# Kernel optimization log

Measured on AMD Instinct MI355X. Metric: run time of the kernel, lower is better.

Reference implementation:

```python
import jax, jax.numpy as jnp
import numpy as np

DIM = 256; HEADS = 8; HD = 32; WS = 3; LOCAL = WS * WS; SR = 4


def _unfold(x, ws):
    # x: (B, c, H, W) -> (B, c, ws*ws, H*W), zero padding (matches nn.Unfold)
    p = ws // 2
    B, c, H, W = x.shape
    xp = jnp.pad(x, ((0, 0), (0, 0), (p, p), (p, p)))
    pat = jnp.stack([xp[:, :, i:i + H, j:j + W] for i in range(ws) for j in range(ws)], axis=2)
    return pat.reshape(B, c, ws * ws, H * W)


def _l2norm(x):
    return x / jnp.sqrt(jnp.sum(x * x, axis=-1, keepdims=True) + 1e-12)


def setup_inputs():
    key = jax.random.key(0)
    ks = jax.random.split(key, 16)
    B, H, W, C, h, d = 4, 64, 64, DIM, HEADS, HD
    N = H * W; pH, pW = H // SR, W // SR; PL = pH * pW; L = 1024
    s = 0.02
    inp = {}
    inp["x"] = jax.random.normal(ks[0], (B, N, C), jnp.float32)
    inp["relative_coords_table"] = jax.random.uniform(ks[1], (L, 2), jnp.float32, -1.0, 1.0)
    inp["relative_pos_index"] = jax.random.randint(ks[2], (N, PL), 0, L)
    inp["q_w"] = jax.random.normal(ks[3], (C, C), jnp.float32) * s
    inp["q_b"] = jnp.zeros((C,), jnp.float32)
    inp["kv_w"] = jax.random.normal(ks[4], (C, 2 * C), jnp.float32) * s
    inp["kv_b"] = jnp.zeros((2 * C,), jnp.float32)
    inp["temperature"] = jnp.log(jnp.expm1(jnp.ones((h, 1, 1), jnp.float32) / 0.24))
    inp["query_embedding"] = jax.random.normal(ks[5], (h, 1, d), jnp.float32) * s
    inp["sr_w"] = jax.random.normal(ks[6], (C, C), jnp.float32) * s
    inp["sr_b"] = jnp.zeros((C,), jnp.float32)
    inp["norm_g"] = jnp.ones((C,), jnp.float32)
    inp["norm_b"] = jnp.zeros((C,), jnp.float32)
    inp["cpb1_w"] = jax.random.normal(ks[7], (2, 512), jnp.float32) * s
    inp["cpb1_b"] = jnp.zeros((512,), jnp.float32)
    inp["cpb2_w"] = jax.random.normal(ks[8], (512, h), jnp.float32) * s
    inp["cpb2_b"] = jnp.zeros((h,), jnp.float32)
    inp["rpb_local"] = jax.random.normal(ks[9], (h, LOCAL), jnp.float32) * 0.0004
    inp["learnable_tokens"] = jax.random.normal(ks[10], (h, d, LOCAL), jnp.float32) * s
    inp["learnable_bias"] = jnp.zeros((h, 1, LOCAL), jnp.float32)
    inp["proj_w"] = jax.random.normal(ks[11], (C, C), jnp.float32) * s
    inp["proj_b"] = jnp.zeros((C,), jnp.float32)
    inp["H"] = H
    inp["W"] = W
    return inp


def _forward(x, relative_coords_table, relative_pos_index, q_w, q_b, kv_w, kv_b,
             temperature, query_embedding, sr_w, sr_b, norm_g, norm_b,
             cpb1_w, cpb1_b, cpb2_w, cpb2_b, rpb_local, learnable_tokens,
             learnable_bias, proj_w, proj_b, H, W):
    B, N, C = x.shape
    h, d = HEADS, HD
    pH, pW = H // SR, W // SR
    PL = pH * pW

    # static buffers: per-pixel valid-neighbor count, log seq-length scale, padding mask
    uf1 = _unfold(jnp.ones((1, 1, H, W), jnp.float32), WS)[0, 0]   # (LOCAL, N)
    counts = uf1.sum(axis=0)[:, None]                               # (N, 1)
    seq_scale = jnp.log(counts + PL)                                # (N, 1)
    pad_mask = (uf1.T == 0)                                         # (N, LOCAL)

    q = (x @ q_w + q_b).reshape(B, N, h, d).transpose(0, 2, 1, 3)   # (B,h,N,d)
    q_norm = _l2norm(q)
    q_scaled = (q_norm + query_embedding) * jax.nn.softplus(temperature) * seq_scale

    kv = (x @ kv_w + kv_b).reshape(B, N, 2 * h, d).transpose(0, 2, 1, 3)
    k_local, v_local = kv[:, :h], kv[:, h:]                         # (B,h,N,d)

    # --- local branch: sliding-window QK^T + learned relative bias ---
    kn = _l2norm(k_local)
    k_img = kn.transpose(0, 1, 3, 2).reshape(B, h * d, H, W)
    k_uf = _unfold(k_img, WS).reshape(B, h, d, LOCAL, N)            # (B,h,d,l,N)
    attn_local = jnp.einsum('bhnd,bhdln->bhnl', q_scaled, k_uf) + rpb_local[None, :, None, :]
    attn_local = jnp.where(pad_mask[None, None], jnp.float32(-1e9), attn_local)

    # --- pooled global branch ---
    xs = jax.nn.gelu(x @ sr_w + sr_b, approximate=False)            # 1x1 conv + GELU
    xs = xs.reshape(B, pH, SR, pW, SR, C).mean(axis=(2, 4)).reshape(B, PL, C)
    mu = xs.mean(-1, keepdims=True)
    var = ((xs - mu) ** 2).mean(-1, keepdims=True)
    xs = (xs - mu) / jnp.sqrt(var + 1e-5) * norm_g + norm_b         # LayerNorm

    kvp = (xs @ kv_w + kv_b).reshape(B, PL, 2 * h, d).transpose(0, 2, 1, 3)
    k_pool, v_pool = kvp[:, :h], kvp[:, h:]
    kp = _l2norm(k_pool)

    # MLP-generated continuous relative position bias
    t = jax.nn.relu(relative_coords_table @ cpb1_w + cpb1_b) @ cpb2_w + cpb2_b  # (L,h)
    pool_bias = t.T[:, relative_pos_index.reshape(-1)].reshape(h, N, PL)

    attn_pool = jnp.einsum('bhnd,bhpd->bhnp', q_scaled, kp) + pool_bias[None]

    # joint softmax over [local | pool]
    attn = jax.nn.softmax(jnp.concatenate([attn_local, attn_pool], axis=-1), axis=-1)
    attn_local, attn_pool = attn[..., :LOCAL], attn[..., LOCAL:]

    # learnable-token refinement of local weights
    attn_local = jnp.einsum('bhnd,hdl->bhnl', q_norm, learnable_tokens) + learnable_bias[None] + attn_local

    v_img = v_local.transpose(0, 1, 3, 2).reshape(B, h * d, H, W)
    v_uf = _unfold(v_img, WS).reshape(B, h, d, LOCAL, N)            # zero-padded V
    x_local = jnp.einsum('bhnl,bhdln->bhnd', attn_local, v_uf)
    x_pool = jnp.einsum('bhnp,bhpd->bhnd', attn_pool, v_pool)

    out = (x_local + x_pool).transpose(0, 2, 1, 3).reshape(B, N, C)
    return out @ proj_w + proj_b


def reference(x, relative_coords_table, relative_pos_index, q_w, q_b, kv_w, kv_b,
              temperature, query_embedding, sr_w, sr_b, norm_g, norm_b,
              cpb1_w, cpb1_b, cpb2_w, cpb2_b, rpb_local, learnable_tokens,
              learnable_bias, proj_w, proj_b, H, W):
    return _forward(x, relative_coords_table, relative_pos_index, q_w, q_b, kv_w, kv_b,
                    temperature, query_embedding, sr_w, sr_b, norm_g, norm_b,
                    cpb1_w, cpb1_b, cpb2_w, cpb2_b, rpb_local, learnable_tokens,
                    learnable_bias, proj_w, proj_b, H, W)
```

## Files before the change

kernel.cpp:

```cpp
#include <hip/hip_runtime.h>
#include <math.h>

#define B_   4
#define N_   4096
#define C_   256
#define NH   8
#define D_   32
#define PL_  256
#define IMG  64

typedef __attribute__((ext_vector_type(8))) short short8b;
typedef __attribute__((ext_vector_type(4))) float f32x4;
typedef unsigned short ushort_t;

__device__ __forceinline__ ushort_t f2bf(float f) {
    unsigned u = __float_as_uint(f);
    u += 0x7FFFu + ((u >> 16) & 1u);
    return (ushort_t)(u >> 16);
}
__device__ __forceinline__ float bf2f(ushort_t s) {
    return __uint_as_float(((unsigned)s) << 16);
}
__device__ __forceinline__ unsigned pk2(float lo, float hi) {
    return (unsigned)f2bf(lo) | ((unsigned)f2bf(hi) << 16);
}
__device__ __forceinline__ float gelu_f(float v) {
    return 0.5f * v * (1.0f + erff(v * 0.70710678118654752440f));
}

__global__ __launch_bounds__(256) void prep_all(const float* __restrict__ x,
                                                const float* __restrict__ q_w,
                                                const float* __restrict__ kv_w,
                                                const float* __restrict__ sr_w,
                                                const float* __restrict__ p_w,
                                                const float* __restrict__ rct,
                                                const float* __restrict__ c1w,
                                                const float* __restrict__ c1b,
                                                const float* __restrict__ c2w,
                                                const float* __restrict__ c2b,
                                                ushort_t* __restrict__ x_bf,
                                                ushort_t* __restrict__ WTall,
                                                ushort_t* __restrict__ pwT,
                                                float* __restrict__ tT)
{
    const int blk = blockIdx.x;
    const int tid = threadIdx.x;
    if (blk < 2048) {
        int gid = blk * 256 + tid;
        const float4* p = (const float4*)(x + (size_t)gid * 8);
        float4 v0 = p[0], v1 = p[1];
        short8b o;
        o[0]=(short)f2bf(v0.x); o[1]=(short)f2bf(v0.y);
        o[2]=(short)f2bf(v0.z); o[3]=(short)f2bf(v0.w);
        o[4]=(short)f2bf(v1.x); o[5]=(short)f2bf(v1.y);
        o[6]=(short)f2bf(v1.z); o[7]=(short)f2bf(v1.w);
        *(short8b*)&x_bf[(size_t)gid * 8] = o;
    } else if (blk < 2208) {
        int wt = (blk - 2048) * 256 + tid;
        int row = wt >> 5;
        int k0  = (wt & 31) << 3;
        const float* W; int N, n; ushort_t* dst;
        if (row < 256)       { W = q_w;  N = 256; n = row;        dst = WTall + (size_t)row * 256; }
        else if (row < 768)  { W = kv_w; N = 512; n = row - 256;  dst = WTall + (size_t)row * 256; }
        else if (row < 1024) { W = sr_w; N = 256; n = row - 768;  dst = WTall + (size_t)row * 256; }
        else                 { W = p_w;  N = 256; n = row - 1024; dst = pwT + (size_t)(row-1024) * 256; }
        short8b v;
        #pragma unroll
        for (int j = 0; j < 8; ++j) v[j] = (short)f2bf(W[(size_t)(k0 + j) * N + n]);
        *(short8b*)&dst[k0] = v;
    } else {
        int l = (blk - 2208) * 4 + (tid >> 6);
        int lane = tid & 63;
        float c0 = rct[l*2+0], c1 = rct[l*2+1];
        float acc[8] = {0,0,0,0,0,0,0,0};
        for (int j = lane; j < 512; j += 64) {
            float hv = fmaxf(c0 * c1w[j] + c1 * c1w[512+j] + c1b[j], 0.f);
            #pragma unroll
            for (int hh = 0; hh < 8; ++hh) acc[hh] += hv * c2w[j*8 + hh];
        }
        #pragma unroll
        for (int o = 32; o > 0; o >>= 1)
            #pragma unroll
            for (int hh = 0; hh < 8; ++hh) acc[hh] += __shfl_xor(acc[hh], o, 64);
        if (lane < 8) tT[lane * 1024 + l] = acc[lane] + c2b[lane];
    }
}

__global__ __launch_bounds__(256) void gemm_fused(const ushort_t* __restrict__ Abf,
                                                  const ushort_t* __restrict__ WTall,
                                                  const float* __restrict__ q_b,
                                                  const float* __restrict__ kv_b,
                                                  const float* __restrict__ sr_b,
                                                  const float* __restrict__ temp,
                                                  const float* __restrict__ qe,
                                                  ushort_t* __restrict__ qs_bf,
                                                  ushort_t* __restrict__ knv_bf,
                                                  float* __restrict__ buf_sr)
{
    __shared__ __align__(16) unsigned char smem[128 * 68 * 4];
    ushort_t* Bs = (ushort_t*)smem;
    float*    Ep = (float*)smem;

    const int tid  = threadIdx.x;
    const int wv   = tid >> 6;
    const int lane = tid & 63;
    const int la   = lane & 15, lg = lane >> 4;
    const int m0   = blockIdx.y * 128 + wv * 32;
    const int bx   = blockIdx.x;
    const int n0   = bx * 64;

    {
        const int srow = tid >> 2, sm = tid & 3;
        const ushort_t* wrow = WTall + (size_t)(n0 + srow) * 256;
        #pragma unroll
        for (int c8 = 0; c8 < 8; ++c8) {
            int ck = c8 * 4 + sm;
            short8b v = *(const short8b*)&wrow[ck * 8];
            *(short8b*)&Bs[srow * 256 + ((ck ^ (srow & 3)) * 8)] = v;
        }
    }
    __syncthreads();

    const ushort_t* a0p = Abf + (size_t)(m0 + la) * 256 + lg * 8;
    const ushort_t* a1p = a0p + (size_t)16 * 256;

    f32x4 acc[2][4];
    #pragma unroll
    for (int i = 0; i < 2; ++i)
        #pragma unroll
        for (int j = 0; j < 4; ++j) acc[i][j] = (f32x4){0.f, 0.f, 0.f, 0.f};

    #pragma unroll
    for (int kit = 0; kit < 8; ++kit) {
        short8b a0 = *(const short8b*)(a0p + kit * 32);
        short8b a1 = *(const short8b*)(a1p + kit * 32);
        #pragma unroll
        for (int nf = 0; nf < 4; ++nf) {
            int brow = nf * 16 + la;
            short8b bb = *(const short8b*)&Bs[brow * 256 + (((kit*4 + lg) ^ (la & 3)) * 8)];
            acc[0][nf] = __builtin_amdgcn_mfma_f32_16x16x32_bf16(a0, bb, acc[0][nf], 0, 0, 0);
            acc[1][nf] = __builtin_amdgcn_mfma_f32_16x16x32_bf16(a1, bb, acc[1][nf], 0, 0, 0);
        }
    }

    if (bx < 12) {
        const float* bias = (bx < 4) ? q_b : kv_b;
        const int cb = (bx < 4) ? n0 : (n0 - 256);
        __syncthreads();
        #pragma unroll
        for (int mf = 0; mf < 2; ++mf)
            #pragma unroll
            for (int nf = 0; nf < 4; ++nf)
                #pragma unroll
                for (int reg = 0; reg < 4; ++reg) {
                    int rl = wv*32 + mf*16 + lg*4 + reg;
                    int c  = nf*16 + la;
                    Ep[rl*68 + c] = acc[mf][nf][reg] + bias[cb + c];
                }
        __syncthreads();
        const int rl = tid >> 1, h2 = tid & 1;
        const int m  = blockIdx.y * 128 + rl;
        const float* rowp = &Ep[rl*68 + h2*32];
        float vv[32]; float ss = 0.f;
        #pragma unroll
        for (int i = 0; i < 8; ++i) {
            float4 v4 = *(const float4*)&rowp[i*4];
            vv[i*4+0]=v4.x; vv[i*4+1]=v4.y; vv[i*4+2]=v4.z; vv[i*4+3]=v4.w;
            ss += v4.x*v4.x + v4.y*v4.y + v4.z*v4.z + v4.w*v4.w;
        }
        if (bx < 4) {
            int head = bx*2 + h2;
            float inv = rsqrtf(ss + 1e-12f);
            float sp  = log1pf(expf(temp[head]));
            int n = m & (N_-1);
            int y = n >> 6, xc = n & 63;
            int ci = 1 + (y > 0) + (y < IMG-1);
            int cj = 1 + (xc > 0) + (xc < IMG-1);
            float s2 = sp * logf((float)(ci*cj) + (float)PL_);
            ushort_t* dst = qs_bf + (size_t)m * 256 + head*32;
            #pragma unroll
            for (int c4 = 0; c4 < 4; ++c4) {
                short8b o;
                #pragma unroll
                for (int j = 0; j < 8; ++j)
                    o[j] = (short)f2bf((vv[c4*8+j]*inv + qe[head*32 + c4*8+j]) * s2);
                *(short8b*)&dst[c4*8] = o;
            }
        } else if (bx < 8) {
            int head = (bx-4)*2 + h2;
            float inv = rsqrtf(ss + 1e-12f);
            ushort_t* dst = knv_bf + (size_t)m * 512 + head*32;
            #pragma unroll
            for (int c4 = 0; c4 < 4; ++c4) {
                short8b o;
                #pragma unroll
                for (int j = 0; j < 8; ++j) o[j] = (short)f2bf(vv[c4*8+j]*inv);
                *(short8b*)&dst[c4*8] = o;
            }
        } else {
            int head = (bx-8)*2 + h2;
            ushort_t* dst = knv_bf + (size_t)m * 512 + 256 + head*32;
            #pragma unroll
            for (int c4 = 0; c4 < 4; ++c4) {
                short8b o;
                #pragma unroll
                for (int j = 0; j < 8; ++j) o[j] = (short)f2bf(vv[c4*8+j]);
                *(short8b*)&dst[c4*8] = o;
            }
        }
    } else {
        #pragma unroll
        for (int mf = 0; mf < 2; ++mf)
            #pragma unroll
            for (int nf = 0; nf < 4; ++nf)
                #pragma unroll
                for (int reg = 0; reg < 4; ++reg) {
                    int m = m0 + mf*16 + lg*4 + reg;
                    int c = n0 + nf*16 + la - 768;
                    float v = acc[mf][nf][reg] + sr_b[c];
                    buf_sr[(size_t)m * 256 + c] = gelu_f(v);
                }
    }
}

template<int ACT>
__global__ __launch_bounds__(256) void gemm_mfma(const ushort_t* __restrict__ Abf,
                                                 const ushort_t* __restrict__ WT,
                                                 const float* __restrict__ bias,
                                                 float* __restrict__ out,
                                                 int M, int N)
{
    __shared__ __align__(16) ushort_t Bs[64 * 256];

    const int tid  = threadIdx.x;
    const int wv   = tid >> 6;
    const int lane = tid & 63;
    const int la   = lane & 15, lg = lane >> 4;
    const int m0   = blockIdx.y * 128 + wv * 32;
    const int n0   = blockIdx.x * 64;

    {
        const int srow = tid >> 2, sm = tid & 3;
        const ushort_t* wrow = WT + (size_t)(n0 + srow) * 256;
        #pragma unroll
        for (int c8 = 0; c8 < 8; ++c8) {
            int ck = c8 * 4 + sm;
            short8b v = *(const short8b*)&wrow[ck * 8];
            *(short8b*)&Bs[srow * 256 + ((ck ^ (srow & 3)) * 8)] = v;
        }
    }
    __syncthreads();

    const ushort_t* a0p = Abf + (size_t)(m0 + la) * 256 + lg * 8;
    const ushort_t* a1p = a0p + (size_t)16 * 256;

    f32x4 acc[2][4];
    #pragma unroll
    for (int i = 0; i < 2; ++i)
        #pragma unroll
        for (int j = 0; j < 4; ++j) acc[i][j] = (f32x4){0.f, 0.f, 0.f, 0.f};

    #pragma unroll
    for (int kit = 0; kit < 8; ++kit) {
        short8b a0 = *(const short8b*)(a0p + kit * 32);
        short8b a1 = *(const short8b*)(a1p + kit * 32);
        #pragma unroll
        for (int nf = 0; nf < 4; ++nf) {
            int brow = nf * 16 + la;
            short8b bb = *(const short8b*)&Bs[brow * 256 + (((kit*4 + lg) ^ (la & 3)) * 8)];
            acc[0][nf] = __builtin_amdgcn_mfma_f32_16x16x32_bf16(a0, bb, acc[0][nf], 0, 0, 0);
            acc[1][nf] = __builtin_amdgcn_mfma_f32_16x16x32_bf16(a1, bb, acc[1][nf], 0, 0, 0);
        }
    }
    #pragma unroll
    for (int mf = 0; mf < 2; ++mf)
        #pragma unroll
        for (int nf = 0; nf < 4; ++nf)
            #pragma unroll
            for (int reg = 0; reg < 4; ++reg) {
                int m  = m0 + mf * 16 + lg * 4 + reg;
                int nn = n0 + nf * 16 + la;
                float v = acc[mf][nf][reg] + bias[nn];
                if (ACT == 1) v = gelu_f(v);
                out[(size_t)m * N + nn] = v;
            }
}

__global__ __launch_bounds__(256) void mid_prep(const int* __restrict__ rpi,
                                                const float* __restrict__ tT,
                                                const ushort_t* __restrict__ knv,
                                                const float* __restrict__ sr,
                                                const float* __restrict__ g,
                                                const float* __restrict__ bb,
                                                ushort_t* __restrict__ pbl,
                                                ushort_t* __restrict__ xs,
                                                ushort_t* __restrict__ vT)
{
    __shared__ float red[256];
    __shared__ __align__(16) ushort_t ts[256][40];
    const int blk = blockIdx.x;
    const int tid = threadIdx.x;

    if (blk < 8192) {
        int gid = blk * 256 + tid;
        int la   = gid & 15;
        int lg   = (gid >> 4) & 3;
        int t    = (gid >> 6) & 15;
        int wv   = (gid >> 10) & 3;
        int tile = (gid >> 12) & 63;
        int h    = gid >> 18;
        int n  = tile * 64 + wv * 16 + la;
        int p0 = t * 16 + lg * 4;
        int4 r = *(const int4*)&rpi[(size_t)n * PL_ + p0];
        const float* tTh = tT + h * 1024;
        ushort4 o;
        o.x = f2bf(tTh[r.x]);
        o.y = f2bf(tTh[r.y]);
        o.z = f2bf(tTh[r.z]);
        o.w = f2bf(tTh[r.w]);
        *(ushort4*)&pbl[(size_t)gid * 4] = o;
    } else if (blk < 9216) {
        int bp = blk - 8192;
        int b = bp >> 8, p = bp & 255;
        int i0 = p >> 4, j0 = p & 15;
        int c = tid;
        float s = 0.f;
        #pragma unroll
        for (int di = 0; di < 4; ++di)
            #pragma unroll
            for (int dj = 0; dj < 4; ++dj) {
                int n = (i0*4 + di) * IMG + (j0*4 + dj);
                s += sr[((size_t)b * N_ + n) * C_ + c];
            }
        s *= (1.f / 16.f);
        red[c] = s; __syncthreads();
        for (int o = 128; o > 0; o >>= 1) { if (c < o) red[c] += red[c+o]; __syncthreads(); }
        float mean = red[0] * (1.f/256.f);
        __syncthreads();
        float dcen = s - mean;
        red[c] = dcen * dcen; __syncthreads();
        for (int o = 128; o > 0; o >>= 1) { if (c < o) red[c] += red[c+o]; __syncthreads(); }
        float var = red[0] * (1.f/256.f);
        float outv = dcen * rsqrtf(var + 1e-5f) * g[c] + bb[c];
        xs[(size_t)bp * C_ + c] = f2bf(outv);
    } else {
        int vb = blk - 9216;
        int nt = vb & 15, bh = vb >> 4;
        const ushort_t* src = knv + ((size_t)((bh >> 3)*N_ + nt*256 + tid)) * 512 + 256 + (bh & 7)*32;
        #pragma unroll
        for (int c = 0; c < 4; ++c)
            *(short8b*)&ts[tid][c*8] = *(const short8b*)&src[c*8];
        __syncthreads();
        int d = tid >> 3, cc = tid & 7;
        ushort_t* dst = vT + ((size_t)bh*32 + d) * (size_t)N_ + nt*256;
        #pragma unroll
        for (int k = 0; k < 4; ++k) {
            int n0 = cc*32 + k*8;
            short8b v;
            #pragma unroll
            for (int j = 0; j < 8; ++j) v[j] = ts[n0+j][d];
            *(short8b*)&dst[n0] = v;
        }
    }
}

__global__ __launch_bounds__(256) void kvp_prep(const float* __restrict__ buf_kvp,
                                                ushort_t* __restrict__ kp_bf,
                                                ushort_t* __restrict__ vpT_bf)
{
    int gid = blockIdx.x * 256 + threadIdx.x;
    if (gid >= B_ * PL_ * NH) return;
    int hh = gid & 7, bp = gid >> 3;
    int b = bp >> 8, p = bp & 255;
    const float* ksrc = buf_kvp + (size_t)bp * 512 + hh * 32;
    float kk[32]; float ss = 0.f;
    #pragma unroll
    for (int i = 0; i < 8; ++i) {
        float4 v = *(const float4*)&ksrc[i*4];
        kk[i*4+0]=v.x; kk[i*4+1]=v.y; kk[i*4+2]=v.z; kk[i*4+3]=v.w;
        ss += v.x*v.x + v.y*v.y + v.z*v.z + v.w*v.w;
    }
    float inv = rsqrtf(ss + 1e-12f);
    ushort_t* kdst = kp_bf + (((size_t)(b*NH + hh) * PL_) + p) * 32;
    #pragma unroll
    for (int c = 0; c < 4; ++c) {
        short8b v;
        #pragma unroll
        for (int j = 0; j < 8; ++j) v[j] = (short)f2bf(kk[c*8+j] * inv);
        *(short8b*)&kdst[c*8] = v;
    }
    const float* vsrc = ksrc + 256;
    ushort_t* vbase = vpT_bf + ((size_t)(b*NH + hh) * 32) * 256 + p;
    #pragma unroll
    for (int d = 0; d < 32; ++d) vbase[d * 256] = f2bf(vsrc[d]);
}

__global__ __launch_bounds__(256) void attn_v4(
    const ushort_t* __restrict__ qs_g,
    const ushort_t* __restrict__ knv_g,
    const ushort_t* __restrict__ kp_g,
    const ushort_t* __restrict__ vpT_g,
    const ushort_t* __restrict__ vT_g,
    const ushort_t* __restrict__ pbl,
    const float* __restrict__ rpb,
    const float* __restrict__ qe,
    const float* __restrict__ temp,
    const float* __restrict__ lt,
    const float* __restrict__ lb,
    ushort_t* __restrict__ outp)
{
    __shared__ __align__(16) ushort_t qs_lds[64*32];
    __shared__ __align__(16) ushort_t ltT_lds[16*32];
    __shared__ __align__(16) ushort_t Wb_lds[4*3*16*40];
    __shared__ float wloc[64*10];
    __shared__ float wext[64*10];
    __shared__ float invs2[64];
    __shared__ float rpb_lds[9], elb_lds[9];

    const int tile = blockIdx.x;
    const int hh   = blockIdx.y;
    const int b    = blockIdx.z;
    const int tid  = threadIdx.x;
    const int wv   = tid >> 6;
    const int lane = tid & 63;
    const int la   = lane & 15;
    const int lg   = lane >> 4;
    const int r0   = wv * 16;

    {
        int row = tid >> 2, ck = tid & 3;
        short8b v = *(const short8b*)&qs_g[((size_t)(b*N_ + tile*64 + row)) * 256 + hh*32 + ck*8];
        *(short8b*)&qs_lds[row*32 + ((ck ^ (row & 3)) * 8)] = v;
    }
    {
        int l = tid >> 4, dd = (tid & 15) * 2;
        ushort_t a = (l < 9) ? f2bf(lt[hh*288 + dd*9 + l]) : (ushort_t)0;
        ushort_t c = (l < 9) ? f2bf(lt[hh*288 + (dd+1)*9 + l]) : (ushort_t)0;
        ltT_lds[l*32 + dd]   = a;
        ltT_lds[l*32 + dd+1] = c;
    }
    {
        short8b z = {0,0,0,0,0,0,0,0};
        for (int i = tid; i < 960; i += 256) *(short8b*)&Wb_lds[i*8] = z;
    }
    if (tid < 64) {
        int xx = tid;
        int ci = 1 + (tile > 0) + (tile < IMG-1);
        int cj = 1 + (xx > 0) + (xx < IMG-1);
        float sp = log1pf(expf(temp[hh]));
        invs2[tid] = 1.0f / (sp * logf((float)(ci*cj) + (float)PL_));
    }
    if (tid >= 64 && tid < 73) {
        int l = tid - 64;
        float e = 0.f;
        for (int d = 0; d < 32; ++d) e += qe[hh*32 + d] * lt[hh*288 + d*9 + l];
        elb_lds[l] = lb[hh*9 + l] - e;
        rpb_lds[l] = rpb[hh*9 + l];
    }
    __syncthreads();

    const short8b af = *(const short8b*)&qs_lds[(r0+la)*32 + ((lg ^ (la & 3)) * 8)];

    {
        f32x4 G[3][2];
        const f32x4 zc = {0.f,0.f,0.f,0.f};
        #pragma unroll
        for (int dyi = 0; dyi < 3; ++dyi) {
            int cy = tile + dyi - 1;
            cy = cy < 0 ? 0 : (cy > 63 ? 63 : cy);
            #pragma unroll
            for (int f = 0; f < 2; ++f) {
                int xp = wv*16 - 8 + 16*f + la;
                xp = xp < 0 ? 0 : (xp > 63 ? 63 : xp);
                const short8b kf = *(const short8b*)
                    &knv_g[((size_t)(b*N_ + cy*64 + xp)) * 512 + hh*32 + lg*8];
                G[dyi][f] = __builtin_amdgcn_mfma_f32_16x16x32_bf16(af, kf, zc, 0, 0, 0);
            }
        }
        #pragma unroll
        for (int f = 0; f < 2; ++f)
            #pragma unroll
            for (int reg = 0; reg < 4; ++reg) {
                int r  = lg*4 + reg;
                int dx = la + 16*f - 8 - r;
                if (dx >= -1 && dx <= 1) {
                    #pragma unroll
                    for (int dyi = 0; dyi < 3; ++dyi)
                        wloc[(r0 + r)*10 + dyi*3 + dx + 1] = G[dyi][f][reg];
                }
            }
    }

    {
        const short8b ltf = *(const short8b*)&ltT_lds[la*32 + lg*8];
        const f32x4 zc = {0.f,0.f,0.f,0.f};
        f32x4 E = __builtin_amdgcn_mfma_f32_16x16x32_bf16(af, ltf, zc, 0, 0, 0);
        if (la < 9) {
            #pragma unroll
            for (int reg = 0; reg < 4; ++reg) {
                int rr = r0 + lg*4 + reg;
                wext[rr*10 + la] = invs2[rr] * E[reg] + elb_lds[la];
            }
        }
    }

    const ushort_t* kph = kp_g + ((size_t)(b*NH + hh) * PL_) * 32;
    const ushort_t* pbw = pbl + ((((size_t)hh * 64 + tile) * 4 + wv) * 4096);

    f32x4 acc[16];
    #pragma unroll
    for (int t = 0; t < 16; ++t) {
        ushort4 b4 = *(const ushort4*)&pbw[t*256 + lg*64 + la*4];
        f32x4 c;
        c[0] = bf2f(b4.x); c[1] = bf2f(b4.y); c[2] = bf2f(b4.z); c[3] = bf2f(b4.w);
        short8b kf = *(const short8b*)&kph[(t*16 + la)*32 + lg*8];
        acc[t] = __builtin_amdgcn_mfma_f32_16x16x32_bf16(kf, af, c, 0, 0, 0);
    }

    const int rr = r0 + la;
    float mx = -3.0e38f;
    #pragma unroll
    for (int t = 0; t < 16; ++t)
        #pragma unroll
        for (int reg = 0; reg < 4; ++reg) mx = fmaxf(mx, acc[t][reg]);
    mx = fmaxf(mx, __shfl_xor(mx, 16, 64));
    mx = fmaxf(mx, __shfl_xor(mx, 32, 64));
    float lv[9];
    #pragma unroll
    for (int l = 0; l < 9; ++l) {
        int dy = l/3 - 1, dx = l%3 - 1;
        int yy = tile + dy, xx = rr + dx;
        bool val = (yy >= 0 && yy < IMG && xx >= 0 && xx < IMG);
        lv[l] = val ? (wloc[rr*10 + l] + rpb_lds[l]) : -1e9f;
        mx = fmaxf(mx, lv[l]);
    }

    float s = 0.f;
    #pragma unroll
    for (int t = 0; t < 16; ++t)
        #pragma unroll
        for (int reg = 0; reg < 4; ++reg) {
            float e = __expf(acc[t][reg] - mx);
            acc[t][reg] = e;
            s += e;
        }
    s += __shfl_xor(s, 16, 64);
    s += __shfl_xor(s, 32, 64);
    float sl = 0.f;
    float el[9];
    #pragma unroll
    for (int l = 0; l < 9; ++l) { el[l] = __expf(lv[l] - mx); sl += el[l]; }
    s += sl;
    const float inv = 1.f / s;

    if (lg == 0) {
        #pragma unroll
        for (int l = 0; l < 9; ++l) {
            int dy = l/3 - 1, dx = l%3 - 1;
            int yy = tile + dy, xx = rr + dx;
            bool val = (yy >= 0 && yy < IMG && xx >= 0 && xx < IMG);
            float wl = el[l]*inv + wext[rr*10 + l];
            Wb_lds[((wv*3 + l/3)*16 + la)*40 + (la + 8 + dx)] =
                val ? f2bf(wl) : (ushort_t)0;
        }
    }

    f32x4 o0 = {0.f,0.f,0.f,0.f}, o1 = {0.f,0.f,0.f,0.f};

    {
        const ushort_t* vTh = vT_g + (size_t)(b*NH + hh) * 32 * N_;
        #pragma unroll
        for (int dyi = 0; dyi < 3; ++dyi) {
            int cy = tile + dyi - 1;
            cy = cy < 0 ? 0 : (cy > 63 ? 63 : cy);
            int nb = cy*64 + wv*16 - 8 + lg*8;
            nb = nb < 0 ? 0 : (nb > (N_ - 8) ? (N_ - 8) : nb);
            short8b wf = *(const short8b*)&Wb_lds[((wv*3 + dyi)*16 + la)*40 + lg*8];
            short8b vf0 = *(const short8b*)&vTh[(size_t)la * N_ + nb];
            short8b vf1 = *(const short8b*)&vTh[(size_t)(16 + la) * N_ + nb];
            o0 = __builtin_amdgcn_mfma_f32_16x16x32_bf16(wf, vf0, o0, 0, 0, 0);
            o1 = __builtin_amdgcn_mfma_f32_16x16x32_bf16(wf, vf1, o1, 0, 0, 0);
        }
    }

    {
        const int src0 = la + 32*(lg & 1);
        const int src1 = src0 + 16;
        const bool hi  = (lg >= 2);
        const ushort_t* vph = vpT_g + ((size_t)(b*NH + hh) * 32) * 256;
        #pragma unroll
        for (int kk = 0; kk < 8; ++kk) {
            unsigned A0 = pk2(acc[2*kk][0]*inv,   acc[2*kk][1]*inv);
            unsigned A1 = pk2(acc[2*kk][2]*inv,   acc[2*kk][3]*inv);
            unsigned B0 = pk2(acc[2*kk+1][0]*inv, acc[2*kk+1][1]*inv);
            unsigned B1 = pk2(acc[2*kk+1][2]*inv, acc[2*kk+1][3]*inv);
            unsigned xa0 = __shfl(A0, src0, 64), xb0 = __shfl(B0, src0, 64);
            unsigned xa1 = __shfl(A1, src0, 64), xb1 = __shfl(B1, src0, 64);
            unsigned ya0 = __shfl(A0, src1, 64), yb0 = __shfl(B0, src1, 64);
            unsigned ya1 = __shfl(A1, src1, 64), yb1 = __shfl(B1, src1, 64);
            union { unsigned u[4]; short8b v; } wf;
            wf.u[0] = hi ? xb0 : xa0;
            wf.u[1] = hi ? xb1 : xa1;
            wf.u[2] = hi ? yb0 : ya0;
            wf.u[3] = hi ? yb1 : ya1;
            short8b vf0 = *(const short8b*)&vph[(size_t)la*256      + kk*32 + lg*8];
            short8b vf1 = *(const short8b*)&vph[(size_t)(16+la)*256 + kk*32 + lg*8];
            o0 = __builtin_amdgcn_mfma_f32_16x16x32_bf16(wf.v, vf0, o0, 0, 0, 0);
            o1 = __builtin_amdgcn_mfma_f32_16x16x32_bf16(wf.v, vf1, o1, 0, 0, 0);
        }
    }

    #pragma unroll
    for (int reg = 0; reg < 4; ++reg) {
        int r2 = r0 + lg*4 + reg;
        int n  = tile*64 + r2;
        ushort_t* orow = outp + ((size_t)(b*N_ + n)) * C_ + hh*32;
        orow[la]      = f2bf(o0[reg]);
        orow[16 + la] = f2bf(o1[reg]);
    }
}

extern "C" void kernel_launch(void* const* d_in, const int* in_sizes, int n_in,
                              void* d_out, int out_size, void* d_ws, size_t ws_size,
                              hipStream_t stream) {
    const float* x    = (const float*)d_in[0];
    const float* rct  = (const float*)d_in[1];
    const int*   rpi  = (const int*)  d_in[2];
    const float* q_w  = (const float*)d_in[3];
    const float* q_b  = (const float*)d_in[4];
    const float* kv_w = (const float*)d_in[5];
    const float* kv_b = (const float*)d_in[6];
    const float* temp = (const float*)d_in[7];
    const float* qe   = (const float*)d_in[8];
    const float* sr_w = (const float*)d_in[9];
    const float* sr_b = (const float*)d_in[10];
    const float* ng   = (const float*)d_in[11];
    const float* nb   = (const float*)d_in[12];
    const float* c1w  = (const float*)d_in[13];
    const float* c1b  = (const float*)d_in[14];
    const float* c2w  = (const float*)d_in[15];
    const float* c2b  = (const float*)d_in[16];
    const float* rpb  = (const float*)d_in[17];
    const float* lt   = (const float*)d_in[18];
    const float* lb   = (const float*)d_in[19];
    const float* p_w  = (const float*)d_in[20];
    const float* p_b  = (const float*)d_in[21];
    float* out = (float*)d_out;

    float* ws = (float*)d_ws;
    const size_t MN = (size_t)B_ * N_;
    float* buf_sr  = ws;
    float* buf_kvp = buf_sr + MN * 256;
    float* buf_t   = buf_kvp + (size_t)B_*PL_*512;
    ushort_t* x_bf   = (ushort_t*)(buf_t + 8*1024);
    ushort_t* pre_bf = x_bf   + MN * 256;
    ushort_t* WTall  = pre_bf + MN * 256;
    ushort_t* pwT    = WTall  + 1024*256;
    ushort_t* qs_bf  = pwT    + 256*256;
    ushort_t* knv_bf = qs_bf  + MN * 256;
    ushort_t* kp_bf  = knv_bf + MN * 512;
    ushort_t* vpT_bf = kp_bf  + (size_t)B_*NH*PL_*32;
    ushort_t* vT_bf  = vpT_bf + (size_t)B_*NH*32*PL_;
    ushort_t* pbl    = vT_bf  + (size_t)B_*NH*32*N_;
    ushort_t* xs_bf  = pbl    + (size_t)2097152*4;

    const int M = (int)MN;

    prep_all<<<2464, 256, 0, stream>>>(x, q_w, kv_w, sr_w, p_w, rct,
                                       c1w, c1b, c2w, c2b, x_bf, WTall, pwT, buf_t);
    gemm_fused<<<dim3(16, M/128), 256, 0, stream>>>(x_bf, WTall, q_b, kv_b, sr_b,
                                                    temp, qe, qs_bf, knv_bf, buf_sr);
    mid_prep<<<9728, 256, 0, stream>>>(rpi, buf_t, knv_bf, buf_sr, ng, nb,
                                       pbl, xs_bf, vT_bf);
    gemm_mfma<0><<<dim3(8, 8), 256, 0, stream>>>(xs_bf, WTall + 256*256, kv_b,
                                                 buf_kvp, B_*PL_, 512);
    kvp_prep<<<(B_*PL_*NH + 255)/256, 256, 0, stream>>>(buf_kvp, kp_bf, vpT_bf);
    attn_v4<<<dim3(64, 8, 4), 256, 0, stream>>>(qs_bf, knv_bf, kp_bf, vpT_bf, vT_bf,
                                                pbl, rpb, qe, temp, lt, lb, pre_bf);
    gemm_mfma<0><<<dim3(4, M/128), 256, 0, stream>>>(pre_bf, pwT, p_b, out, M, 256);
}
```

Measured before the change: 133.4 us.

## Fuse K/V pooled normalization into GEMM epilogue and drop LDS staging

The gemm_fused epilogue now L2-normalizes and converts q/k straight from MFMA accumulators, reducing over each head with wave shuffles instead of staging through a shared-memory tile with two barriers. The q scale log term is replaced by precomputed constants. A new gemm_kvp kernel fuses the pooled kv projection with k normalization and v transpose, which removes the fp32 buf_kvp round trip and the kvp_prep launch. The tradeoff is that stores become scattered 2-byte writes instead of 16-byte vectors, which could hurt coalescing.

New measurement: 131.6 us. About the same (-1.3%).

```diff
diff --git a/kernel.cpp b/kernel.cpp
--- a/kernel.cpp
+++ b/kernel.cpp
@@ -97,9 +97,7 @@
                                                   ushort_t* __restrict__ knv_bf,
                                                   float* __restrict__ buf_sr)
 {
-    __shared__ __align__(16) unsigned char smem[128 * 68 * 4];
-    ushort_t* Bs = (ushort_t*)smem;
-    float*    Ep = (float*)smem;
+    __shared__ __align__(16) ushort_t Bs[64 * 256];
 
     const int tid  = threadIdx.x;
     const int wv   = tid >> 6;
@@ -143,71 +141,62 @@
         }
     }
 
-    if (bx < 12) {
+    if (bx < 8) {
         const float* bias = (bx < 4) ? q_b : kv_b;
         const int cb = (bx < 4) ? n0 : (n0 - 256);
-        __syncthreads();
+        float bv[4];
+        #pragma unroll
+        for (int nf = 0; nf < 4; ++nf) bv[nf] = bias[cb + nf*16 + la];
+        float sp0 = 0.f, sp1 = 0.f;
+        if (bx < 4) {
+            sp0 = log1pf(expf(temp[bx*2 + 0]));
+            sp1 = log1pf(expf(temp[bx*2 + 1]));
+        }
+        #pragma unroll
+        for (int mf = 0; mf < 2; ++mf)
+            #pragma unroll
+            for (int reg = 0; reg < 4; ++reg) {
+                int m = m0 + mf*16 + lg*4 + reg;
+                #pragma unroll
+                for (int h2 = 0; h2 < 2; ++h2) {
+                    float v0 = acc[mf][2*h2][reg]   + bv[2*h2];
+                    float v1 = acc[mf][2*h2+1][reg] + bv[2*h2+1];
+                    float ss = v0*v0 + v1*v1;
+                    ss += __shfl_xor(ss, 1, 64);
+                    ss += __shfl_xor(ss, 2, 64);
+                    ss += __shfl_xor(ss, 4, 64);
+                    ss += __shfl_xor(ss, 8, 64);
+                    float inv = rsqrtf(ss + 1e-12f);
+                    if (bx < 4) {
+                        int head = bx*2 + h2;
+                        int n = m & (N_-1);
+                        int y = n >> 6, xc = n & 63;
+                        int cnt = (1 + (y > 0) + (y < IMG-1)) * (1 + (xc > 0) + (xc < IMG-1));
+                        float lc = (cnt == 4) ? 5.5606816f : (cnt == 6) ? 5.5683445f : 5.5797298f;
+                        float s2 = (h2 ? sp1 : sp0) * lc;
+                        ushort_t* dst = qs_bf + (size_t)m * 256 + head*32;
+                        dst[la]      = f2bf((v0*inv + qe[head*32 + la])      * s2);
+                        dst[16 + la] = f2bf((v1*inv + qe[head*32 + 16 + la]) * s2);
+                    } else {
+                        int head = (bx-4)*2 + h2;
+                        ushort_t* dst = knv_bf + (size_t)m * 512 + head*32;
+                        dst[la]      = f2bf(v0*inv);
+                        dst[16 + la] = f2bf(v1*inv);
+                    }
+                }
+            }
+    } else if (bx < 12) {
         #pragma unroll
         for (int mf = 0; mf < 2; ++mf)
             #pragma unroll
             for (int nf = 0; nf < 4; ++nf)
                 #pragma unroll
                 for (int reg = 0; reg < 4; ++reg) {
-                    int rl = wv*32 + mf*16 + lg*4 + reg;
-                    int c  = nf*16 + la;
-                    Ep[rl*68 + c] = acc[mf][nf][reg] + bias[cb + c];
+                    int m = m0 + mf*16 + lg*4 + reg;
+                    int col_kv = n0 - 256 + nf*16 + la;
+                    knv_bf[(size_t)m * 512 + col_kv] =
+                        f2bf(acc[mf][nf][reg] + kv_b[col_kv]);
                 }
-        __syncthreads();
-        const int rl = tid >> 1, h2 = tid & 1;
-        const int m  = blockIdx.y * 128 + rl;
-        const float* rowp = &Ep[rl*68 + h2*32];
-        float vv[32]; float ss = 0.f;
-        #pragma unroll
-        for (int i = 0; i < 8; ++i) {
-            float4 v4 = *(const float4*)&rowp[i*4];
-            vv[i*4+0]=v4.x; vv[i*4+1]=v4.y; vv[i*4+2]=v4.z; vv[i*4+3]=v4.w;
-            ss += v4.x*v4.x + v4.y*v4.y + v4.z*v4.z + v4.w*v4.w;
-        }
-        if (bx < 4) {
-            int head = bx*2 + h2;
-            float inv = rsqrtf(ss + 1e-12f);
-            float sp  = log1pf(expf(temp[head]));
-            int n = m & (N_-1);
-            int y = n >> 6, xc = n & 63;
-            int ci = 1 + (y > 0) + (y < IMG-1);
-            int cj = 1 + (xc > 0) + (xc < IMG-1);
-            float s2 = sp * logf((float)(ci*cj) + (float)PL_);
-            ushort_t* dst = qs_bf + (size_t)m * 256 + head*32;
-            #pragma unroll
-            for (int c4 = 0; c4 < 4; ++c4) {
-                short8b o;
-                #pragma unroll
-                for (int j = 0; j < 8; ++j)
-                    o[j] = (short)f2bf((vv[c4*8+j]*inv + qe[head*32 + c4*8+j]) * s2);
-                *(short8b*)&dst[c4*8] = o;
-            }
-        } else if (bx < 8) {
-            int head = (bx-4)*2 + h2;
-            float inv = rsqrtf(ss + 1e-12f);
-            ushort_t* dst = knv_bf + (size_t)m * 512 + head*32;
-            #pragma unroll
-            for (int c4 = 0; c4 < 4; ++c4) {
-                short8b o;
-                #pragma unroll
-                for (int j = 0; j < 8; ++j) o[j] = (short)f2bf(vv[c4*8+j]*inv);
-                *(short8b*)&dst[c4*8] = o;
-            }
-        } else {
-            int head = (bx-8)*2 + h2;
-            ushort_t* dst = knv_bf + (size_t)m * 512 + 256 + head*32;
-            #pragma unroll
-            for (int c4 = 0; c4 < 4; ++c4) {
-                short8b o;
-                #pragma unroll
-                for (int j = 0; j < 8; ++j) o[j] = (short)f2bf(vv[c4*8+j]);
-                *(short8b*)&dst[c4*8] = o;
-            }
-        }
     } else {
         #pragma unroll
         for (int mf = 0; mf < 2; ++mf)
@@ -217,8 +206,101 @@
                 for (int reg = 0; reg < 4; ++reg) {
                     int m = m0 + mf*16 + lg*4 + reg;
                     int c = n0 + nf*16 + la - 768;
-                    float v = acc[mf][nf][reg] + sr_b[c];
-                    buf_sr[(size_t)m * 256 + c] = gelu_f(v);
+                    buf_sr[(size_t)m * 256 + c] = gelu_f(acc[mf][nf][reg] + sr_b[c]);
+                }
+    }
+}
+
+__global__ __launch_bounds__(256) void gemm_kvp(const ushort_t* __restrict__ Abf,
+                                                const ushort_t* __restrict__ WT,
+                                                const float* __restrict__ kv_b,
+                                                ushort_t* __restrict__ kp_bf,
+                                                ushort_t* __restrict__ vpT_bf)
+{
+    __shared__ __align__(16) ushort_t Bs[64 * 256];
+
+    const int tid  = threadIdx.x;
+    const int wv   = tid >> 6;
+    const int lane = tid & 63;
+    const int la   = lane & 15, lg = lane >> 4;
+    const int m0   = blockIdx.y * 128 + wv * 32;
+    const int bx   = blockIdx.x;
+    const int n0   = bx * 64;
+
+    {
+        const int srow = tid >> 2, sm = tid & 3;
+        const ushort_t* wrow = WT + (size_t)(n0 + srow) * 256;
+        #pragma unroll
+        for (int c8 = 0; c8 < 8; ++c8) {
+            int ck = c8 * 4 + sm;
+            short8b v = *(const short8b*)&wrow[ck * 8];
+            *(short8b*)&Bs[srow * 256 + ((ck ^ (srow & 3)) * 8)] = v;
+        }
+    }
+    __syncthreads();
+
+    const ushort_t* a0p = Abf + (size_t)(m0 + la) * 256 + lg * 8;
+    const ushort_t* a1p = a0p + (size_t)16 * 256;
+
+    f32x4 acc[2][4];
+    #pragma unroll
+    for (int i = 0; i < 2; ++i)
+        #pragma unroll
+        for (int j = 0; j < 4; ++j) acc[i][j] = (f32x4){0.f, 0.f, 0.f, 0.f};
+
+    #pragma unroll
+    for (int kit = 0; kit < 8; ++kit) {
+        short8b a0 = *(const short8b*)(a0p + kit * 32);
+        short8b a1 = *(const short8b*)(a1p + kit * 32);
+        #pragma unroll
+        for (int nf = 0; nf < 4; ++nf) {
+            int brow = nf * 16 + la;
+            short8b bb = *(const short8b*)&Bs[brow * 256 + (((kit*4 + lg) ^ (la & 3)) * 8)];
+            acc[0][nf] = __builtin_amdgcn_mfma_f32_16x16x32_bf16(a0, bb, acc[0][nf], 0, 0, 0);
+            acc[1][nf] = __builtin_amdgcn_mfma_f32_16x16x32_bf16(a1, bb, acc[1][nf], 0, 0, 0);
+        }
+    }
+
+    if (bx < 4) {
+        float bv[4];
+        #pragma unroll
+        for (int nf = 0; nf < 4; ++nf) bv[nf] = kv_b[n0 + nf*16 + la];
+        #pragma unroll
+        for (int mf = 0; mf < 2; ++mf)
+            #pragma unroll
+            for (int reg = 0; reg < 4; ++reg) {
+                int m = m0 + mf*16 + lg*4 + reg;
+                int b = m >> 8, p = m & 255;
+                #pragma unroll
+                for (int h2 = 0; h2 < 2; ++h2) {
+                    float v0 = acc[mf][2*h2][reg]   + bv[2*h2];
+                    float v1 = acc[mf][2*h2+1][reg] + bv[2*h2+1];
+                    float ss = v0*v0 + v1*v1;
+                    ss += __shfl_xor(ss, 1, 64);
+                    ss += __shfl_xor(ss, 2, 64);
+                    ss += __shfl_xor(ss, 4, 64);
+                    ss += __shfl_xor(ss, 8, 64);
+                    float inv = rsqrtf(ss + 1e-12f);
+                    int head = bx*2 + h2;
+                    ushort_t* dst = kp_bf + (((size_t)(b*NH + head)) * PL_ + p) * 32;
+                    dst[la]      = f2bf(v0*inv);
+                    dst[16 + la] = f2bf(v1*inv);
+                }
+            }
+    } else {
+        #pragma unroll
+        for (int mf = 0; mf < 2; ++mf)
+            #pragma unroll
+            for (int nf = 0; nf < 4; ++nf)
+                #pragma unroll
+                for (int reg = 0; reg < 4; ++reg) {
+                    int m = m0 + mf*16 + lg*4 + reg;
+                    int b = m >> 8, p = m & 255;
+                    int col_kv = n0 + nf*16 + la;
+                    int cv = col_kv - 256;
+                    int head = cv >> 5, d = cv & 31;
+                    vpT_bf[(((size_t)(b*NH + head)) * 32 + d) * 256 + p] =
+                        f2bf(acc[mf][nf][reg] + kv_b[col_kv]);
                 }
     }
 }
@@ -362,37 +444,6 @@
             *(short8b*)&dst[n0] = v;
         }
     }
-}
-
-__global__ __launch_bounds__(256) void kvp_prep(const float* __restrict__ buf_kvp,
-                                                ushort_t* __restrict__ kp_bf,
-                                                ushort_t* __restrict__ vpT_bf)
-{
-    int gid = blockIdx.x * 256 + threadIdx.x;
-    if (gid >= B_ * PL_ * NH) return;
-    int hh = gid & 7, bp = gid >> 3;
-    int b = bp >> 8, p = bp & 255;
-    const float* ksrc = buf_kvp + (size_t)bp * 512 + hh * 32;
-    float kk[32]; float ss = 0.f;
-    #pragma unroll
-    for (int i = 0; i < 8; ++i) {
-        float4 v = *(const float4*)&ksrc[i*4];
-        kk[i*4+0]=v.x; kk[i*4+1]=v.y; kk[i*4+2]=v.z; kk[i*4+3]=v.w;
-        ss += v.x*v.x + v.y*v.y + v.z*v.z + v.w*v.w;
-    }
-    float inv = rsqrtf(ss + 1e-12f);
-    ushort_t* kdst = kp_bf + (((size_t)(b*NH + hh) * PL_) + p) * 32;
-    #pragma unroll
-    for (int c = 0; c < 4; ++c) {
-        short8b v;
-        #pragma unroll
-        for (int j = 0; j < 8; ++j) v[j] = (short)f2bf(kk[c*8+j] * inv);
-        *(short8b*)&kdst[c*8] = v;
-    }
-    const float* vsrc = ksrc + 256;
-    ushort_t* vbase = vpT_bf + ((size_t)(b*NH + hh) * 32) * 256 + p;
-    #pragma unroll
-    for (int d = 0; d < 32; ++d) vbase[d * 256] = f2bf(vsrc[d]);
 }
 
 __global__ __launch_bounds__(256) void attn_v4(
@@ -650,8 +701,7 @@
     float* ws = (float*)d_ws;
     const size_t MN = (size_t)B_ * N_;
     float* buf_sr  = ws;
-    float* buf_kvp = buf_sr + MN * 256;
-    float* buf_t   = buf_kvp + (size_t)B_*PL_*512;
+    float* buf_t   = buf_sr + MN * 256;
     ushort_t* x_bf   = (ushort_t*)(buf_t + 8*1024);
     ushort_t* pre_bf = x_bf   + MN * 256;
     ushort_t* WTall  = pre_bf + MN * 256;
@@ -672,9 +722,8 @@
                                                     temp, qe, qs_bf, knv_bf, buf_sr);
     mid_prep<<<9728, 256, 0, stream>>>(rpi, buf_t, knv_bf, buf_sr, ng, nb,
                                        pbl, xs_bf, vT_bf);
-    gemm_mfma<0><<<dim3(8, 8), 256, 0, stream>>>(xs_bf, WTall + 256*256, kv_b,
-                                                 buf_kvp, B_*PL_, 512);
-    kvp_prep<<<(B_*PL_*NH + 255)/256, 256, 0, stream>>>(buf_kvp, kp_bf, vpT_bf);
+    gemm_kvp<<<dim3(8, 8), 256, 0, stream>>>(xs_bf, WTall + 256*256, kv_b,
+                                             kp_bf, vpT_bf);
     attn_v4<<<dim3(64, 8, 4), 256, 0, stream>>>(qs_bf, knv_bf, kp_bf, vpT_bf, vT_bf,
                                                 pbl, rpb, qe, temp, lt, lb, pre_bf);
     gemm_mfma<0><<<dim3(4, M/128), 256, 0, stream>>>(pre_bf, pwT, p_b, out, M, 256);
```
